# Performance work log

Measured on AMD Instinct MI355X. Metric: run time of the kernel, lower is better.

The kernel has to match this reference:

```python
import jax, jax.numpy as jnp
import numpy as np

B, S, D, H = 4, 2048, 512, 8
DK = D // H


def setup_inputs() -> dict:
    key = jax.random.key(0)
    ks = jax.random.split(key, 11)
    scale = 1.0 / np.sqrt(D)
    inp = {
        'q': jax.random.normal(ks[0], (B, S, D), jnp.float32),
        'k': jax.random.normal(ks[1], (B, S, D), jnp.float32),
        'v': jax.random.normal(ks[2], (B, S, D), jnp.float32),
        'mask': jnp.tril(jnp.ones((S, S), jnp.int32))[None, None, :, :],  # [1,1,S,S] causal
        'w_q': jax.random.normal(ks[3], (D, D), jnp.float32) * scale,
        'b_q': jnp.zeros((D,), jnp.float32),
        'w_k': jax.random.normal(ks[4], (D, D), jnp.float32) * scale,
        'b_k': jnp.zeros((D,), jnp.float32),
        'w_v': jax.random.normal(ks[5], (D, D), jnp.float32) * scale,
        'b_v': jnp.zeros((D,), jnp.float32),
        'w_o': jax.random.normal(ks[6], (D, D), jnp.float32) * scale,
        'b_o': jnp.zeros((D,), jnp.float32),
    }
    return inp


def reference(q, k, v, mask, w_q, b_q, w_k, b_k, w_v, b_v, w_o, b_o):
    # QKV projections (nn.Linear: x @ W^T + b)
    def split_heads(x):  # [B,S,D] -> [B,H,S,DK]
        return x.reshape(B, S, H, DK).transpose(0, 2, 1, 3)

    qh = split_heads(q @ w_q.T + b_q)
    kh = split_heads(k @ w_k.T + b_k)
    vh = split_heads(v @ w_v.T + b_v)

    scores = jnp.einsum('bhqd,bhkd->bhqk', qh, kh) / jnp.sqrt(jnp.float32(DK))
    scores = jnp.where(mask == 0, jnp.float32(-1e9), scores)
    attn = jax.nn.softmax(scores, axis=-1)  # dropout is identity in eval
    ctx = jnp.einsum('bhqk,bhkd->bhqd', attn, vh)  # [B,H,S,DK]
    ctx = ctx.transpose(0, 2, 1, 3).reshape(B, S, D)
    return ctx @ w_o.T + b_o
```

## Files before the change

kernel.cpp:

```cpp
#include <hip/hip_runtime.h>
#include <hip/hip_bf16.h>


#define BATCH  4
#define SLEN   2048
#define DMODEL 512
#define NHEAD  8
#define DHEAD  64
#define MROWS  (BATCH * SLEN)

#define NQ ((size_t)MROWS * DMODEL)
#define NW ((size_t)DMODEL * DMODEL)
#define NB ((size_t)DMODEL)
#define CVT_TOTAL (3 * NQ + 4 * NW + 4 * NB)

#define SCALE_L2E 0.180336880f

typedef short bf16x8 __attribute__((ext_vector_type(8)));
typedef float f32x4  __attribute__((ext_vector_type(4)));

typedef unsigned int __attribute__((address_space(1))) glb_u32_t;
typedef unsigned int __attribute__((address_space(3))) lds_u32_t;

__device__ __forceinline__ void async_copy16(const unsigned short* g, unsigned short* l) {
    __builtin_amdgcn_global_load_lds((glb_u32_t*)g, (lds_u32_t*)l, 16, 0, 0);
}

__device__ __forceinline__ float bf2f(unsigned short u) {
    union { unsigned int i; float f; } v; v.i = ((unsigned int)u) << 16; return v.f;
}
__device__ __forceinline__ unsigned short f2bf(float f) {
    union { float f; unsigned int i; } v; v.f = f;
    unsigned int x = v.i;
    return (unsigned short)((x + 0x7fffu + ((x >> 16) & 1u)) >> 16);
}
__device__ __forceinline__ unsigned int pkbf(float a, float b) {
    union { __hip_bfloat162 h; unsigned int u; } cv;
    cv.h = __float22bfloat162_rn(float2{a, b});
    return cv.u;
}

__device__ __forceinline__ void wait0_barrier() {
    asm volatile("s_waitcnt vmcnt(0)" ::: "memory");
    __builtin_amdgcn_s_barrier();
    asm volatile("" ::: "memory");
}

__global__ __launch_bounds__(256)
void cvt_kernel(const float* __restrict__ q, const float* __restrict__ k,
                const float* __restrict__ v,
                const float* __restrict__ wq, const float* __restrict__ wk,
                const float* __restrict__ wv, const float* __restrict__ wo,
                const float* __restrict__ bq, const float* __restrict__ bk,
                const float* __restrict__ bv, const float* __restrict__ bo,
                unsigned short* __restrict__ dst)
{
    const size_t i4 = ((size_t)blockIdx.x * 256 + threadIdx.x) * 4;
    if (i4 >= CVT_TOTAL) return;
    const float* src;
    size_t off;
    if      (i4 <     NQ)          { src = q;  off = i4; }
    else if (i4 < 2 * NQ)          { src = k;  off = i4 - NQ; }
    else if (i4 < 3 * NQ)          { src = v;  off = i4 - 2 * NQ; }
    else if (i4 < 3 * NQ + NW)     { src = wq; off = i4 - 3 * NQ; }
    else if (i4 < 3 * NQ + 2 * NW) { src = wk; off = i4 - 3 * NQ - NW; }
    else if (i4 < 3 * NQ + 3 * NW) { src = wv; off = i4 - 3 * NQ - 2 * NW; }
    else if (i4 < 3 * NQ + 4 * NW) { src = wo; off = i4 - 3 * NQ - 3 * NW; }
    else if (i4 < 3 * NQ + 4 * NW + NB)     { src = bq; off = i4 - 3 * NQ - 4 * NW; }
    else if (i4 < 3 * NQ + 4 * NW + 2 * NB) { src = bk; off = i4 - 3 * NQ - 4 * NW - NB; }
    else if (i4 < 3 * NQ + 4 * NW + 3 * NB) { src = bv; off = i4 - 3 * NQ - 4 * NW - 2 * NB; }
    else                                    { src = bo; off = i4 - 3 * NQ - 4 * NW - 3 * NB; }
    const float4 f = *(const float4*)(src + off);
    ushort4 o;
    o.x = f2bf(f.x); o.y = f2bf(f.y); o.z = f2bf(f.z); o.w = f2bf(f.w);
    *(ushort4*)(dst + i4) = o;
}

template <typename OutT>
__device__ __forceinline__ void gemm_body(const unsigned short* __restrict__ A,
                                          const unsigned short* __restrict__ W,
                                          const unsigned short* __restrict__ bias,
                                          OutT* __restrict__ C, int mode)
{
    __shared__ __align__(16) unsigned short As[2][128 * 32];
    __shared__ __align__(16) unsigned short Bs[2][128 * 32];

    const int tid  = threadIdx.x;
    const int wave = tid >> 6;
    const int lane = tid & 63;
    const int l15  = lane & 15;
    const int quad = lane >> 4;
    const int m0   = blockIdx.x * 128;
    const int n0   = blockIdx.y * 128;
    const int wm   = (wave & 1) * 64;
    const int wn   = (wave >> 1) * 64;
    const int srow = lane >> 2;
    const int scol = (((lane & 3) ^ (srow & 3)) * 8);
    const int rsw  = (quad ^ (l15 & 3)) * 8;

    auto stage = [&](int k0, int buf) {
        async_copy16(A + (size_t)(m0 + wave * 16 + srow) * DMODEL + k0 + scol, As[buf] + wave * 512);
        async_copy16(A + (size_t)(m0 + (wave + 4) * 16 + srow) * DMODEL + k0 + scol, As[buf] + (wave + 4) * 512);
        async_copy16(W + (size_t)(n0 + wave * 16 + srow) * DMODEL + k0 + scol, Bs[buf] + wave * 512);
        async_copy16(W + (size_t)(n0 + (wave + 4) * 16 + srow) * DMODEL + k0 + scol, Bs[buf] + (wave + 4) * 512);
    };

    f32x4 acc[4][4] = {};
    stage(0, 0);

    #pragma unroll 1
    for (int kt = 0; kt < 16; kt++) {
        const int cur = kt & 1;
        wait0_barrier();
        if (kt < 15) stage((kt + 1) * 32, cur ^ 1);

        bf16x8 af[4], bfr[4];
        #pragma unroll
        for (int i = 0; i < 4; i++)
            af[i] = *(const bf16x8*)(As[cur] + (wm + i * 16 + l15) * 32 + rsw);
        #pragma unroll
        for (int j = 0; j < 4; j++)
            bfr[j] = *(const bf16x8*)(Bs[cur] + (wn + j * 16 + l15) * 32 + rsw);
        #pragma unroll
        for (int i = 0; i < 4; i++)
            #pragma unroll
            for (int j = 0; j < 4; j++)
                acc[i][j] = __builtin_amdgcn_mfma_f32_16x16x32_bf16(af[i], bfr[j], acc[i][j], 0, 0, 0);
    }

    if (mode == 2) {
        #pragma unroll
        for (int j = 0; j < 4; j++) {
            const int col = n0 + wn + j * 16 + l15;
            const float bv = bf2f(bias[col]);
            const int hh = col >> 6, dk = col & 63;
            #pragma unroll
            for (int i = 0; i < 4; i++) {
                const int row = m0 + wm + i * 16 + quad * 4;
                const int bb = row >> 11, s = row & 2047;
                uint2 o2;
                o2.x = pkbf(acc[i][j][0] + bv, acc[i][j][1] + bv);
                o2.y = pkbf(acc[i][j][2] + bv, acc[i][j][3] + bv);
                *(uint2*)((unsigned short*)C + ((size_t)((bb * NHEAD + hh) * DHEAD + dk)) * SLEN + s) = o2;
            }
        }
    } else {
        const float oscale = (mode == 0) ? SCALE_L2E : 1.0f;
        #pragma unroll
        for (int j = 0; j < 4; j++) {
            const int col = n0 + wn + j * 16 + l15;
            const float bv = bf2f(bias[col]);
            #pragma unroll
            for (int i = 0; i < 4; i++) {
                const int row = m0 + wm + i * 16 + quad * 4;
                #pragma unroll
                for (int r = 0; r < 4; r++) {
                    const float val = (acc[i][j][r] + bv) * oscale;
                    if constexpr (sizeof(OutT) == 4)
                        C[(size_t)(row + r) * DMODEL + col] = val;
                    else
                        C[(size_t)(row + r) * DMODEL + col] = f2bf(val);
                }
            }
        }
    }
}

__global__ __launch_bounds__(256, 3)
void qkv_gemm_kernel(const unsigned short* __restrict__ qin,
                     const unsigned short* __restrict__ kin,
                     const unsigned short* __restrict__ vin,
                     const unsigned short* __restrict__ wq,
                     const unsigned short* __restrict__ bq,
                     const unsigned short* __restrict__ wk,
                     const unsigned short* __restrict__ bk,
                     const unsigned short* __restrict__ wv,
                     const unsigned short* __restrict__ bv,
                     unsigned short* __restrict__ qh,
                     unsigned short* __restrict__ kh,
                     unsigned short* __restrict__ vt)
{
    const int z = blockIdx.z;
    const unsigned short* A    = (z == 0) ? qin : (z == 1) ? kin : vin;
    const unsigned short* W    = (z == 0) ? wq  : (z == 1) ? wk  : wv;
    const unsigned short* bias = (z == 0) ? bq  : (z == 1) ? bk  : bv;
    unsigned short*       C    = (z == 0) ? qh  : (z == 1) ? kh  : vt;
    gemm_body<unsigned short>(A, W, bias, C, z);
}

__global__ __launch_bounds__(256, 3)
void oproj_gemm_kernel(const unsigned short* __restrict__ ctx,
                       const unsigned short* __restrict__ wo,
                       const unsigned short* __restrict__ bo,
                       float* __restrict__ out)
{
    gemm_body<float>(ctx, wo, bo, out, 3);
}

__global__ __launch_bounds__(256, 2)
void attn_kernel(const unsigned short* __restrict__ qh,
                 const unsigned short* __restrict__ kh,
                 const unsigned short* __restrict__ vt,
                 unsigned short* __restrict__ ctx)
{
    __shared__ __align__(16) unsigned short Ks[2][64 * 64];
    __shared__ __align__(16) unsigned short Vs[2][64 * 64];
    __shared__ __align__(16) unsigned short Ps[4 * 2 * 16 * 64];

    const int tid  = threadIdx.x;
    const int wave = tid >> 6;
    const int lane = tid & 63;
    const int l15  = lane & 15;
    const int quad = lane >> 4;

    const int bh = blockIdx.x;
    const int x  = blockIdx.y;
    const int g  = (x < 8) ? x : 23 - x;
    const int qta = g;
    const int qtb = 31 - g;
    const int b  = bh >> 3;
    const int h  = bh & 7;

    const size_t base = (size_t)b * SLEN * DMODEL + (size_t)h * DHEAD;
    const unsigned short* Q  = qh + base;
    const unsigned short* K  = kh + base;
    const unsigned short* VT = vt + (size_t)bh * DHEAD * SLEN;

    const int krow_l = lane >> 3;
    const int kcol_l = ((lane & 7) ^ (krow_l & 7)) * 8;

    const int qrow_a = qta * 64 + wave * 16 + l15;
    const int qrow_b = qtb * 64 + wave * 16 + l15;
    const bf16x8 qa0 = *(const bf16x8*)(Q + (size_t)qrow_a * DMODEL + quad * 8);
    const bf16x8 qa1 = *(const bf16x8*)(Q + (size_t)qrow_a * DMODEL + 32 + quad * 8);
    const bf16x8 qb0 = *(const bf16x8*)(Q + (size_t)qrow_b * DMODEL + quad * 8);
    const bf16x8 qb1 = *(const bf16x8*)(Q + (size_t)qrow_b * DMODEL + 32 + quad * 8);

    f32x4 oacc_a[4] = {};
    f32x4 oacc_b[4] = {};
    float lsum_a = 0.0f, lsum_b = 0.0f;

    unsigned short* Pa = Ps + (wave * 2 + 0) * (16 * 64);
    unsigned short* Pb = Ps + (wave * 2 + 1) * (16 * 64);

    auto stageKV = [&](int kt, int buf) {
        async_copy16(K + (size_t)(kt * 64 + wave * 8 + krow_l) * DMODEL + kcol_l,
                     Ks[buf] + wave * 512);
        async_copy16(K + (size_t)(kt * 64 + (wave + 4) * 8 + krow_l) * DMODEL + kcol_l,
                     Ks[buf] + (wave + 4) * 512);
        async_copy16(VT + (size_t)(wave * 8 + krow_l) * SLEN + kt * 64 + kcol_l,
                     Vs[buf] + wave * 512);
        async_copy16(VT + (size_t)((wave + 4) * 8 + krow_l) * SLEN + kt * 64 + kcol_l,
                     Vs[buf] + (wave + 4) * 512);
    };

    auto softmax_pack = [&](f32x4* sacc, unsigned short* Pw, float& lsum) {
        #pragma unroll
        for (int j = 0; j < 4; j++) {
            const float p0 = exp2f(sacc[j][0]);
            const float p1 = exp2f(sacc[j][1]);
            const float p2v = exp2f(sacc[j][2]);
            const float p3 = exp2f(sacc[j][3]);
            lsum += (p0 + p1) + (p2v + p3);
            uint2 pw;
            pw.x = pkbf(p0, p1);
            pw.y = pkbf(p2v, p3);
            const int chunk = (j * 2 + (quad >> 1)) ^ (l15 & 7);
            *(uint2*)(Pw + l15 * 64 + chunk * 8 + (quad & 1) * 4) = pw;
        }
    };

    auto diag_mask = [&](f32x4* sacc, int kt, int qrow) {
        #pragma unroll
        for (int j = 0; j < 4; j++)
            #pragma unroll
            for (int r = 0; r < 4; r++) {
                const int kv = kt * 64 + j * 16 + quad * 4 + r;
                if (kv > qrow) sacc[j][r] = -1e30f;
            }
    };

    const int nkt = 32 - g;
    stageKV(0, 0);

    #pragma unroll 1
    for (int kt = 0; kt < nkt; kt++) {
        const int cur = kt & 1;
        wait0_barrier();
        if (kt + 1 < nkt) stageKV(kt + 1, cur ^ 1);

        if (kt <= g) {
            f32x4 sa[4] = {}, sb[4] = {};
            #pragma unroll
            for (int kk = 0; kk < 2; kk++) {
                const bf16x8 qfa = kk ? qa1 : qa0;
                const bf16x8 qfb = kk ? qb1 : qb0;
                #pragma unroll
                for (int j = 0; j < 4; j++) {
                    bf16x8 kf = *(const bf16x8*)(Ks[cur] + (j * 16 + l15) * 64
                                                    + (((kk * 4 + quad) ^ (l15 & 7)) * 8));
                    sb[j] = __builtin_amdgcn_mfma_f32_16x16x32_bf16(kf, qfb, sb[j], 0, 0, 0);
                    sa[j] = __builtin_amdgcn_mfma_f32_16x16x32_bf16(kf, qfa, sa[j], 0, 0, 0);
                }
            }
            if (kt == qta) diag_mask(sa, kt, qrow_a);
            softmax_pack(sa, Pa, lsum_a);
            softmax_pack(sb, Pb, lsum_b);
            asm volatile("s_waitcnt lgkmcnt(0)" ::: "memory");

            #pragma unroll
            for (int kk = 0; kk < 2; kk++) {
                bf16x8 pfa = *(const bf16x8*)(Pa + l15 * 64 + (((kk * 4 + quad) ^ (l15 & 7)) * 8));
                bf16x8 pfb = *(const bf16x8*)(Pb + l15 * 64 + (((kk * 4 + quad) ^ (l15 & 7)) * 8));
                #pragma unroll
                for (int jd = 0; jd < 4; jd++) {
                    bf16x8 vf = *(const bf16x8*)(Vs[cur] + (jd * 16 + l15) * 64
                                                    + (((kk * 4 + quad) ^ (l15 & 7)) * 8));
                    oacc_a[jd] = __builtin_amdgcn_mfma_f32_16x16x32_bf16(vf, pfa, oacc_a[jd], 0, 0, 0);
                    oacc_b[jd] = __builtin_amdgcn_mfma_f32_16x16x32_bf16(vf, pfb, oacc_b[jd], 0, 0, 0);
                }
            }
        } else {
            f32x4 sb[4] = {};
            #pragma unroll
            for (int kk = 0; kk < 2; kk++) {
                const bf16x8 qfb = kk ? qb1 : qb0;
                #pragma unroll
                for (int j = 0; j < 4; j++) {
                    bf16x8 kf = *(const bf16x8*)(Ks[cur] + (j * 16 + l15) * 64
                                                    + (((kk * 4 + quad) ^ (l15 & 7)) * 8));
                    sb[j] = __builtin_amdgcn_mfma_f32_16x16x32_bf16(kf, qfb, sb[j], 0, 0, 0);
                }
            }
            if (kt == qtb) diag_mask(sb, kt, qrow_b);
            softmax_pack(sb, Pb, lsum_b);
            asm volatile("s_waitcnt lgkmcnt(0)" ::: "memory");

            #pragma unroll
            for (int kk = 0; kk < 2; kk++) {
                bf16x8 pfb = *(const bf16x8*)(Pb + l15 * 64 + (((kk * 4 + quad) ^ (l15 & 7)) * 8));
                #pragma unroll
                for (int jd = 0; jd < 4; jd++) {
                    bf16x8 vf = *(const bf16x8*)(Vs[cur] + (jd * 16 + l15) * 64
                                                    + (((kk * 4 + quad) ^ (l15 & 7)) * 8));
                    oacc_b[jd] = __builtin_amdgcn_mfma_f32_16x16x32_bf16(vf, pfb, oacc_b[jd], 0, 0, 0);
                }
            }
        }
    }

    {
        float la = lsum_a;
        la += __shfl_xor(la, 16, 64);
        la += __shfl_xor(la, 32, 64);
        const float invla = 1.0f / la;
        #pragma unroll
        for (int jd = 0; jd < 4; jd++) {
            uint2 o2;
            o2.x = pkbf(oacc_a[jd][0] * invla, oacc_a[jd][1] * invla);
            o2.y = pkbf(oacc_a[jd][2] * invla, oacc_a[jd][3] * invla);
            *(uint2*)(ctx + base + (size_t)qrow_a * DMODEL + jd * 16 + quad * 4) = o2;
        }
    }
    {
        float lb = lsum_b;
        lb += __shfl_xor(lb, 16, 64);
        lb += __shfl_xor(lb, 32, 64);
        const float invlb = 1.0f / lb;
        #pragma unroll
        for (int jd = 0; jd < 4; jd++) {
            uint2 o2;
            o2.x = pkbf(oacc_b[jd][0] * invlb, oacc_b[jd][1] * invlb);
            o2.y = pkbf(oacc_b[jd][2] * invlb, oacc_b[jd][3] * invlb);
            *(uint2*)(ctx + base + (size_t)qrow_b * DMODEL + jd * 16 + quad * 4) = o2;
        }
    }
}

extern "C" void kernel_launch(void* const* d_in, const int* in_sizes, int n_in,
                              void* d_out, int out_size, void* d_ws, size_t ws_size,
                              hipStream_t stream)
{
    const float* q   = (const float*)d_in[0];
    const float* k   = (const float*)d_in[1];
    const float* v   = (const float*)d_in[2];
    const float* w_q = (const float*)d_in[4];
    const float* b_q = (const float*)d_in[5];
    const float* w_k = (const float*)d_in[6];
    const float* b_k = (const float*)d_in[7];
    const float* w_v = (const float*)d_in[8];
    const float* b_v = (const float*)d_in[9];
    const float* w_o = (const float*)d_in[10];
    const float* b_o = (const float*)d_in[11];
    float* out = (float*)d_out;

    unsigned short* ws = (unsigned short*)d_ws;
    unsigned short* qb  = ws;
    unsigned short* kb  = ws + NQ;
    unsigned short* vb  = ws + 2 * NQ;
    unsigned short* wqb = ws + 3 * NQ;
    unsigned short* wkb = wqb + NW;
    unsigned short* wvb = wkb + NW;
    unsigned short* wob = wvb + NW;
    unsigned short* bqb = wob + NW;
    unsigned short* bkb = bqb + NB;
    unsigned short* bvb = bkb + NB;
    unsigned short* bob = bvb + NB;
    unsigned short* qh  = bob + NB;
    unsigned short* kh  = qh + NQ;
    unsigned short* vt  = kh + NQ;
    unsigned short* ctx = vt + NQ;

    dim3 blk(256);
    hipLaunchKernelGGL(cvt_kernel, dim3((unsigned)(CVT_TOTAL / 4 / 256)), blk, 0, stream,
                       q, k, v, w_q, w_k, w_v, w_o, b_q, b_k, b_v, b_o, ws);
    hipLaunchKernelGGL(qkv_gemm_kernel, dim3(MROWS / 128, DMODEL / 128, 3), blk, 0, stream,
                       qb, kb, vb, wqb, bqb, wkb, bkb, wvb, bvb, qh, kh, vt);
    hipLaunchKernelGGL(attn_kernel, dim3(BATCH * NHEAD, 16), blk, 0, stream,
                       qh, kh, vt, ctx);
    hipLaunchKernelGGL(oproj_gemm_kernel, dim3(MROWS / 128, DMODEL / 128), blk, 0, stream,
                       ctx, wob, bob, out);
}
```

Before: 198.7 us.

## Fuse fp32-to-bf16 activation conversion into QKV GEMM and retile output projection

The separate conversion pass over the q/k/v activations is removed. The QKV GEMM now loads fp32 rows directly into registers, packs them to bf16 and writes them into swizzled LDS, with the next tile's global load overlapped with the MFMA work, so the extra round trip through HBM for the activations goes away. The output projection is rewritten with 64x64 tiles and 128-thread blocks to launch more blocks and fill the device better. In exchange, the register-staged A path adds VGPR pressure and a vmcnt wait inside the loop, replacing the asynchronous LDS copy.

```diff
diff --git a/kernel.cpp b/kernel.cpp
--- a/kernel.cpp
+++ b/kernel.cpp
@@ -12,7 +12,7 @@
 #define NQ ((size_t)MROWS * DMODEL)
 #define NW ((size_t)DMODEL * DMODEL)
 #define NB ((size_t)DMODEL)
-#define CVT_TOTAL (3 * NQ + 4 * NW + 4 * NB)
+#define CVTW_TOTAL (4 * NW + 4 * NB)
 
 #define SCALE_L2E 0.180336880f
 
@@ -47,40 +47,34 @@
 }
 
 __global__ __launch_bounds__(256)
-void cvt_kernel(const float* __restrict__ q, const float* __restrict__ k,
-                const float* __restrict__ v,
-                const float* __restrict__ wq, const float* __restrict__ wk,
-                const float* __restrict__ wv, const float* __restrict__ wo,
-                const float* __restrict__ bq, const float* __restrict__ bk,
-                const float* __restrict__ bv, const float* __restrict__ bo,
-                unsigned short* __restrict__ dst)
+void cvt_w_kernel(const float* __restrict__ wq, const float* __restrict__ wk,
+                  const float* __restrict__ wv, const float* __restrict__ wo,
+                  const float* __restrict__ bq, const float* __restrict__ bk,
+                  const float* __restrict__ bv, const float* __restrict__ bo,
+                  unsigned short* __restrict__ dst)
 {
     const size_t i4 = ((size_t)blockIdx.x * 256 + threadIdx.x) * 4;
-    if (i4 >= CVT_TOTAL) return;
+    if (i4 >= CVTW_TOTAL) return;
     const float* src;
     size_t off;
-    if      (i4 <     NQ)          { src = q;  off = i4; }
-    else if (i4 < 2 * NQ)          { src = k;  off = i4 - NQ; }
-    else if (i4 < 3 * NQ)          { src = v;  off = i4 - 2 * NQ; }
-    else if (i4 < 3 * NQ + NW)     { src = wq; off = i4 - 3 * NQ; }
-    else if (i4 < 3 * NQ + 2 * NW) { src = wk; off = i4 - 3 * NQ - NW; }
-    else if (i4 < 3 * NQ + 3 * NW) { src = wv; off = i4 - 3 * NQ - 2 * NW; }
-    else if (i4 < 3 * NQ + 4 * NW) { src = wo; off = i4 - 3 * NQ - 3 * NW; }
-    else if (i4 < 3 * NQ + 4 * NW + NB)     { src = bq; off = i4 - 3 * NQ - 4 * NW; }
-    else if (i4 < 3 * NQ + 4 * NW + 2 * NB) { src = bk; off = i4 - 3 * NQ - 4 * NW - NB; }
-    else if (i4 < 3 * NQ + 4 * NW + 3 * NB) { src = bv; off = i4 - 3 * NQ - 4 * NW - 2 * NB; }
-    else                                    { src = bo; off = i4 - 3 * NQ - 4 * NW - 3 * NB; }
+    if      (i4 <     NW)          { src = wq; off = i4; }
+    else if (i4 < 2 * NW)          { src = wk; off = i4 - NW; }
+    else if (i4 < 3 * NW)          { src = wv; off = i4 - 2 * NW; }
+    else if (i4 < 4 * NW)          { src = wo; off = i4 - 3 * NW; }
+    else if (i4 < 4 * NW + NB)     { src = bq; off = i4 - 4 * NW; }
+    else if (i4 < 4 * NW + 2 * NB) { src = bk; off = i4 - 4 * NW - NB; }
+    else if (i4 < 4 * NW + 3 * NB) { src = bv; off = i4 - 4 * NW - 2 * NB; }
+    else                           { src = bo; off = i4 - 4 * NW - 3 * NB; }
     const float4 f = *(const float4*)(src + off);
     ushort4 o;
     o.x = f2bf(f.x); o.y = f2bf(f.y); o.z = f2bf(f.z); o.w = f2bf(f.w);
     *(ushort4*)(dst + i4) = o;
 }
 
-template <typename OutT>
-__device__ __forceinline__ void gemm_body(const unsigned short* __restrict__ A,
-                                          const unsigned short* __restrict__ W,
-                                          const unsigned short* __restrict__ bias,
-                                          OutT* __restrict__ C, int mode)
+__device__ __forceinline__ void gemm_body_f32(const float* __restrict__ A,
+                                              const unsigned short* __restrict__ W,
+                                              const unsigned short* __restrict__ bias,
+                                              unsigned short* __restrict__ C, int mode)
 {
     __shared__ __align__(16) unsigned short As[2][128 * 32];
     __shared__ __align__(16) unsigned short Bs[2][128 * 32];
@@ -98,21 +92,48 @@
     const int scol = (((lane & 3) ^ (srow & 3)) * 8);
     const int rsw  = (quad ^ (l15 & 3)) * 8;
 
-    auto stage = [&](int k0, int buf) {
-        async_copy16(A + (size_t)(m0 + wave * 16 + srow) * DMODEL + k0 + scol, As[buf] + wave * 512);
-        async_copy16(A + (size_t)(m0 + (wave + 4) * 16 + srow) * DMODEL + k0 + scol, As[buf] + (wave + 4) * 512);
+    const int arow = lane >> 2;
+    const int achk = lane & 3;
+    const int gchk = achk ^ (arow & 3);
+    const int ar0  = m0 + wave * 16 + arow;
+    const int ar1  = m0 + (wave + 4) * 16 + arow;
+
+    f32x4 a0, a1, a2, a3;
+    auto loadA = [&](int k0) {
+        const float* p0 = A + (size_t)ar0 * DMODEL + k0 + gchk * 8;
+        const float* p1 = A + (size_t)ar1 * DMODEL + k0 + gchk * 8;
+        a0 = *(const f32x4*)(p0);
+        a1 = *(const f32x4*)(p0 + 4);
+        a2 = *(const f32x4*)(p1);
+        a3 = *(const f32x4*)(p1 + 4);
+    };
+    auto writeA = [&](int buf) {
+        uint4 w0, w1;
+        w0.x = pkbf(a0[0], a0[1]); w0.y = pkbf(a0[2], a0[3]);
+        w0.z = pkbf(a1[0], a1[1]); w0.w = pkbf(a1[2], a1[3]);
+        w1.x = pkbf(a2[0], a2[1]); w1.y = pkbf(a2[2], a2[3]);
+        w1.z = pkbf(a3[0], a3[1]); w1.w = pkbf(a3[2], a3[3]);
+        *(uint4*)(As[buf] + (wave * 16 + arow) * 32 + achk * 8) = w0;
+        *(uint4*)(As[buf] + ((wave + 4) * 16 + arow) * 32 + achk * 8) = w1;
+    };
+    auto stageW = [&](int k0, int buf) {
         async_copy16(W + (size_t)(n0 + wave * 16 + srow) * DMODEL + k0 + scol, Bs[buf] + wave * 512);
         async_copy16(W + (size_t)(n0 + (wave + 4) * 16 + srow) * DMODEL + k0 + scol, Bs[buf] + (wave + 4) * 512);
     };
 
     f32x4 acc[4][4] = {};
-    stage(0, 0);
+    stageW(0, 0);
+    loadA(0);
+    asm volatile("s_waitcnt vmcnt(0)" ::: "memory");
+    writeA(0);
 
     #pragma unroll 1
     for (int kt = 0; kt < 16; kt++) {
         const int cur = kt & 1;
-        wait0_barrier();
-        if (kt < 15) stage((kt + 1) * 32, cur ^ 1);
+        asm volatile("s_waitcnt lgkmcnt(0)" ::: "memory");
+        __builtin_amdgcn_s_barrier();
+        asm volatile("" ::: "memory");
+        if (kt < 15) { stageW((kt + 1) * 32, cur ^ 1); loadA((kt + 1) * 32); }
 
         bf16x8 af[4], bfr[4];
         #pragma unroll
@@ -126,6 +147,11 @@
             #pragma unroll
             for (int j = 0; j < 4; j++)
                 acc[i][j] = __builtin_amdgcn_mfma_f32_16x16x32_bf16(af[i], bfr[j], acc[i][j], 0, 0, 0);
+
+        if (kt < 15) {
+            asm volatile("s_waitcnt vmcnt(0)" ::: "memory");
+            writeA(cur ^ 1);
+        }
     }
 
     if (mode == 2) {
@@ -154,22 +180,17 @@
             for (int i = 0; i < 4; i++) {
                 const int row = m0 + wm + i * 16 + quad * 4;
                 #pragma unroll
-                for (int r = 0; r < 4; r++) {
-                    const float val = (acc[i][j][r] + bv) * oscale;
-                    if constexpr (sizeof(OutT) == 4)
-                        C[(size_t)(row + r) * DMODEL + col] = val;
-                    else
-                        C[(size_t)(row + r) * DMODEL + col] = f2bf(val);
-                }
+                for (int r = 0; r < 4; r++)
+                    C[(size_t)(row + r) * DMODEL + col] = f2bf((acc[i][j][r] + bv) * oscale);
             }
         }
     }
 }
 
 __global__ __launch_bounds__(256, 3)
-void qkv_gemm_kernel(const unsigned short* __restrict__ qin,
-                     const unsigned short* __restrict__ kin,
-                     const unsigned short* __restrict__ vin,
+void qkv_gemm_kernel(const float* __restrict__ qin,
+                     const float* __restrict__ kin,
+                     const float* __restrict__ vin,
                      const unsigned short* __restrict__ wq,
                      const unsigned short* __restrict__ bq,
                      const unsigned short* __restrict__ wk,
@@ -181,20 +202,80 @@
                      unsigned short* __restrict__ vt)
 {
     const int z = blockIdx.z;
-    const unsigned short* A    = (z == 0) ? qin : (z == 1) ? kin : vin;
+    const float*          A    = (z == 0) ? qin : (z == 1) ? kin : vin;
     const unsigned short* W    = (z == 0) ? wq  : (z == 1) ? wk  : wv;
     const unsigned short* bias = (z == 0) ? bq  : (z == 1) ? bk  : bv;
     unsigned short*       C    = (z == 0) ? qh  : (z == 1) ? kh  : vt;
-    gemm_body<unsigned short>(A, W, bias, C, z);
-}
-
-__global__ __launch_bounds__(256, 3)
+    gemm_body_f32(A, W, bias, C, z);
+}
+
+__global__ __launch_bounds__(128, 4)
 void oproj_gemm_kernel(const unsigned short* __restrict__ ctx,
                        const unsigned short* __restrict__ wo,
                        const unsigned short* __restrict__ bo,
                        float* __restrict__ out)
 {
-    gemm_body<float>(ctx, wo, bo, out, 3);
+    __shared__ __align__(16) unsigned short As[2][64 * 32];
+    __shared__ __align__(16) unsigned short Bs[2][64 * 32];
+
+    const int tid  = threadIdx.x;
+    const int wave = tid >> 6;
+    const int lane = tid & 63;
+    const int l15  = lane & 15;
+    const int quad = lane >> 4;
+    const int m0   = blockIdx.x * 64;
+    const int n0   = blockIdx.y * 64;
+    const int wm   = wave * 32;
+    const int srow = lane >> 2;
+    const int scol = (((lane & 3) ^ (srow & 3)) * 8);
+    const int rsw  = (quad ^ (l15 & 3)) * 8;
+
+    auto stage = [&](int k0, int buf) {
+        async_copy16(ctx + (size_t)(m0 + wave * 32 + srow) * DMODEL + k0 + scol,
+                     As[buf] + (wave * 2) * 512);
+        async_copy16(ctx + (size_t)(m0 + wave * 32 + 16 + srow) * DMODEL + k0 + scol,
+                     As[buf] + (wave * 2 + 1) * 512);
+        async_copy16(wo + (size_t)(n0 + wave * 32 + srow) * DMODEL + k0 + scol,
+                     Bs[buf] + (wave * 2) * 512);
+        async_copy16(wo + (size_t)(n0 + wave * 32 + 16 + srow) * DMODEL + k0 + scol,
+                     Bs[buf] + (wave * 2 + 1) * 512);
+    };
+
+    f32x4 acc[2][4] = {};
+    stage(0, 0);
+
+    #pragma unroll 1
+    for (int kt = 0; kt < 16; kt++) {
+        const int cur = kt & 1;
+        wait0_barrier();
+        if (kt < 15) stage((kt + 1) * 32, cur ^ 1);
+
+        bf16x8 af[2], bfr[4];
+        #pragma unroll
+        for (int i = 0; i < 2; i++)
+            af[i] = *(const bf16x8*)(As[cur] + (wm + i * 16 + l15) * 32 + rsw);
+        #pragma unroll
+        for (int j = 0; j < 4; j++)
+            bfr[j] = *(const bf16x8*)(Bs[cur] + (j * 16 + l15) * 32 + rsw);
+        #pragma unroll
+        for (int i = 0; i < 2; i++)
+            #pragma unroll
+            for (int j = 0; j < 4; j++)
+                acc[i][j] = __builtin_amdgcn_mfma_f32_16x16x32_bf16(af[i], bfr[j], acc[i][j], 0, 0, 0);
+    }
+
+    #pragma unroll
+    for (int j = 0; j < 4; j++) {
+        const int col = n0 + j * 16 + l15;
+        const float bv = bf2f(bo[col]);
+        #pragma unroll
+        for (int i = 0; i < 2; i++) {
+            const int row = m0 + wm + i * 16 + quad * 4;
+            #pragma unroll
+            for (int r = 0; r < 4; r++)
+                out[(size_t)(row + r) * DMODEL + col] = acc[i][j][r] + bv;
+        }
+    }
 }
 
 __global__ __launch_bounds__(256, 2)
@@ -395,9 +476,6 @@
     float* out = (float*)d_out;
 
     unsigned short* ws = (unsigned short*)d_ws;
-    unsigned short* qb  = ws;
-    unsigned short* kb  = ws + NQ;
-    unsigned short* vb  = ws + 2 * NQ;
     unsigned short* wqb = ws + 3 * NQ;
     unsigned short* wkb = wqb + NW;
     unsigned short* wvb = wkb + NW;
@@ -412,12 +490,12 @@
     unsigned short* ctx = vt + NQ;
 
     dim3 blk(256);
-    hipLaunchKernelGGL(cvt_kernel, dim3((unsigned)(CVT_TOTAL / 4 / 256)), blk, 0, stream,
-                       q, k, v, w_q, w_k, w_v, w_o, b_q, b_k, b_v, b_o, ws);
+    hipLaunchKernelGGL(cvt_w_kernel, dim3((unsigned)(CVTW_TOTAL / 4 / 256)), blk, 0, stream,
+                       w_q, w_k, w_v, w_o, b_q, b_k, b_v, b_o, wqb);
     hipLaunchKernelGGL(qkv_gemm_kernel, dim3(MROWS / 128, DMODEL / 128, 3), blk, 0, stream,
-                       qb, kb, vb, wqb, bqb, wkb, bkb, wvb, bvb, qh, kh, vt);
+                       q, k, v, wqb, bqb, wkb, bkb, wvb, bvb, qh, kh, vt);
     hipLaunchKernelGGL(attn_kernel, dim3(BATCH * NHEAD, 16), blk, 0, stream,
                        qh, kh, vt, ctx);
-    hipLaunchKernelGGL(oproj_gemm_kernel, dim3(MROWS / 128, DMODEL / 128), blk, 0, stream,
+    hipLaunchKernelGGL(oproj_gemm_kernel, dim3(MROWS / 64, DMODEL / 64), dim3(128), 0, stream,
                        ctx, wob, bob, out);
 }
```

New measurement: 199.6 us. About the same (+0.5%).
